# Optimization experiments

Measured on AMD Instinct MI355X. Metric: run time of the kernel, lower is better.

Reference implementation:

```python
import jax, jax.numpy as jnp
import numpy as np

PAD = 4
MAX_DISP = 4


def setup_inputs() -> dict:
    key = jax.random.key(0)
    k1, k2 = jax.random.split(key)
    in1 = jax.random.normal(k1, (8, 256, 128, 128), dtype=jnp.float32)
    in2 = jax.random.normal(k2, (8, 256, 128, 128), dtype=jnp.float32)
    return {"in1": in1, "in2": in2}


def reference(in1, in2):
    # in1, in2: [B, C, H, W]
    H, W = in1.shape[2], in1.shape[3]
    in2_pad = jnp.pad(in2, ((0, 0), (0, 0), (PAD, PAD), (PAD, PAD)))
    D = 2 * MAX_DISP + 1  # 9 displacements per axis -> 81 output channels
    outs = []
    # torch.meshgrid('ij') + zip(offsetx, offsety): dy is the outer (slow) index,
    # dx the inner (fast) index.
    for dy in range(D):
        for dx in range(D):
            # mean over channel dim of elementwise product with shifted window
            corr = jnp.mean(in1 * in2_pad[:, :, dy:dy + H, dx:dx + W],
                            axis=1, keepdims=True)  # [B,1,H,W]
            outs.append(corr)
    return jnp.concatenate(outs, axis=1)  # [B, D*D, H, W]
```

## Files before the change

kernel.cpp:

```cpp
#include <hip/hip_runtime.h>


#define B_   8
#define C_   256
#define H_   128
#define W_   128
#define ND   9
#define TY   16
#define TW   16
#define CS   (H_ * W_)
#define NST  32
#define S2SLOT 18432
#define S1SLOT 8192
#define S1OFF  55296
#define FOFF   79872
#define FAOFF  116736
#define LDS_TOTAL 133120

typedef short v8s __attribute__((ext_vector_type(8)));
typedef float v4f __attribute__((ext_vector_type(4)));

__device__ __forceinline__ unsigned short f2bf(float f) {
    union { float f; unsigned u; } v; v.f = f;
    return (unsigned short)((v.u + 0x7FFFu + ((v.u >> 16) & 1u)) >> 16);
}

__device__ __forceinline__ void dma16(const float* g, void* lds) {
    __builtin_amdgcn_global_load_lds(
        (const __attribute__((address_space(1))) void*)g,
        (__attribute__((address_space(3))) void*)lds, 16, 0, 0);
}

#define FENCE()     asm volatile("" ::: "memory")
#define WAITK2_BAR() do {                                                         \
        if (w >= 2 && w < 8) asm volatile("s_waitcnt vmcnt(2)\n\ts_barrier" ::: "memory"); \
        else                 asm volatile("s_waitcnt vmcnt(4)\n\ts_barrier" ::: "memory"); \
    } while (0)
#define WAITK1_BAR() do {                                                         \
        if (w >= 2 && w < 8) asm volatile("s_waitcnt vmcnt(1)\n\ts_barrier" ::: "memory"); \
        else                 asm volatile("s_waitcnt vmcnt(2)\n\ts_barrier" ::: "memory"); \
    } while (0)
#define WAITV0_BAR() asm volatile("s_waitcnt vmcnt(0)\n\ts_barrier" ::: "memory")
#define LGKM0_BAR()  asm volatile("s_waitcnt lgkmcnt(0)\n\ts_barrier" ::: "memory")
#define LGKM0()      asm volatile("s_waitcnt lgkmcnt(0)" ::: "memory")

__global__ __launch_bounds__(1024, 4)
void corr_mfma_kernel(const float* __restrict__ in1,
                      const float* __restrict__ in2,
                      float* __restrict__ out) {
    extern __shared__ __align__(16) char ldsbase[];
    float* S2 = (float*)ldsbase;
    float* S1 = (float*)(ldsbase + S1OFF);
    short* F  = (short*)(ldsbase + FOFF);
    short* FA = (short*)(ldsbase + FAOFF);
    float* EP = (float*)ldsbase;

    const int tid  = threadIdx.x;
    const int lane = tid & 63;
    const int w    = tid >> 6;

    const int lin = blockIdx.x;
    const int b   = lin & 7;
    const int idx = lin >> 3;
    const int x0  = (idx & 7) * TW;
    const int y0  = (idx >> 3) * TY;

    const int i_px = lane & 15;
    const int kb   = lane >> 4;

    const float* dsrc[2];
    int ddst[2];
    #pragma unroll
    for (int t = 0; t < 2; ++t) {
        if (t == 1 && w >= 2) { dsrc[t] = in2; ddst[t] = 0; continue; }
        const int q   = (w < 2) ? (w * 2 + t) : (4 + (w - 2));
        const int g   = q * 64 + lane;
        const int ch  = g / 144;
        const int rem = g % 144;
        const int r   = rem / 6;
        const int jg  = rem % 6;
        int gy = y0 - 4 + r;
        int gx = x0 - 4 + jg * 4;
        gy = gy < 0 ? 0 : (gy > H_ - 1 ? H_ - 1 : gy);
        gx = gx < 0 ? 0 : (gx > W_ - 4 ? W_ - 4 : gx);
        dsrc[t] = in2 + ((long)(b * C_) + ch) * CS + gy * W_ + gx;
        ddst[t] = q * 1024;
    }
    const float* d1src = in2;
    int d1dst = 0;
    if (w >= 8) {
        const int q   = w - 8;
        const int g   = q * 64 + lane;
        const int ch  = g >> 6;
        const int rem = g & 63;
        const int r   = rem >> 2;
        const int xg  = rem & 3;
        d1src = in1 + ((long)(b * C_) + ch) * CS + (y0 + r) * W_ + x0 + xg * 4;
        d1dst = q * 1024;
    }

    const bool c2act = (tid < 576);
    const int  crr   = tid / 24, cjj = tid % 24;
    const bool c2val = c2act && ((unsigned)(y0 - 4 + crr) < (unsigned)H_) &&
                                ((unsigned)(x0 - 4 + cjj) < (unsigned)W_);
    const bool c1act = (tid < 256);

    v4f acc0[ND];
    v4f acc1[5];
    #pragma unroll
    for (int d = 0; d < ND; ++d) acc0[d] = (v4f)0.0f;
    #pragma unroll
    for (int p = 0; p < 5; ++p)  acc1[p] = (v4f)0.0f;

#define ISSUE_G(s_) do {                                                      \
        const long so = (long)(s_) * 8 * CS;                                  \
        char* sb2 = (char*)S2 + ((s_) % 3) * S2SLOT;                          \
        dma16(dsrc[0] + so, sb2 + ddst[0]);                                   \
        if (w < 2) dma16(dsrc[1] + so, sb2 + ddst[1]);                        \
        if (w >= 8)                                                           \
            dma16(d1src + so, (char*)ldsbase + S1OFF + ((s_) % 3) * S1SLOT + d1dst); \
        FENCE();                                                              \
    } while (0)

#define CONVERT(s_) do {                                                      \
        if (c2act) {                                                          \
            const float* sh = S2 + ((s_) % 3) * 4608;                         \
            v8s pk;                                                           \
            _Pragma("unroll")                                                 \
            for (int e = 0; e < 8; ++e)                                       \
                pk[e] = (short)f2bf(sh[e * 576 + tid]);                       \
            if (!c2val) pk = (v8s)0;                                          \
            *(v8s*)&F[(((s_) & 3) * 576 + tid) * 8] = pk;                     \
        }                                                                     \
        if (c1act) {                                                          \
            const float* sa = S1 + ((s_) % 3) * 2048;                         \
            v8s pa;                                                           \
            _Pragma("unroll")                                                 \
            for (int e = 0; e < 8; ++e)                                       \
                pa[e] = (short)f2bf(sa[e * 256 + tid]);                       \
            *(v8s*)&FA[tid * 32 + ((s_) & 3) * 8] = pa;                       \
        }                                                                     \
    } while (0)

    ISSUE_G(0);
    ISSUE_G(1);
    ISSUE_G(2);
    WAITK2_BAR();
    CONVERT(0);
    LGKM0_BAR();

    #pragma unroll
    for (int s = 0; s < NST; ++s) {
        if (s + 3 < NST) ISSUE_G(s + 3);

        if ((s & 3) == 3) {
            const v8s af = *(const v8s*)&FA[w * 512 + i_px * 32 + kb * 8];
            #pragma unroll
            for (int dy = 0; dy < ND; ++dy) {
                const int rj = (w + dy) * 24 + i_px;
                const v8s f = *(const v8s*)&F[kb * 4608 + (rj << 3)];
                acc0[dy] = __builtin_amdgcn_mfma_f32_16x16x32_bf16(
                    af, f, acc0[dy], 0, 0, 0);
            }
            const int hi = i_px >> 3, j1 = 16 + (i_px & 7);
            #pragma unroll
            for (int P = 0; P < 5; ++P) {
                int r = w + 2 * P + hi;
                if (r > 23) r = 23;
                const int rj = r * 24 + j1;
                const v8s f = *(const v8s*)&F[kb * 4608 + (rj << 3)];
                acc1[P] = __builtin_amdgcn_mfma_f32_16x16x32_bf16(
                    af, f, acc1[P], 0, 0, 0);
            }
        }

        if (s + 3 < NST)       { WAITK2_BAR(); }
        else if (s == NST - 3) { WAITK1_BAR(); }
        else if (s == NST - 2) { WAITV0_BAR(); }

        if (s < NST - 1) {
            CONVERT(s + 1);
            LGKM0_BAR();
        }
    }

    float* epw = EP + w * 384;
    const int g4 = lane >> 4;
    #pragma unroll
    for (int dy = 0; dy < ND; ++dy) {
        #pragma unroll
        for (int q = 0; q < 4; ++q)
            epw[(g4 * 4 + q) * 24 + i_px] = acc0[dy][q];
        if ((i_px >> 3) == (dy & 1)) {
            #pragma unroll
            for (int q = 0; q < 4; ++q)
                epw[(g4 * 4 + q) * 24 + 16 + (i_px & 7)] = acc1[dy >> 1][q];
        }
        LGKM0();
        #pragma unroll
        for (int rep = 0; rep < 3; ++rep) {
            const int dx = g4 + rep * 4;
            if (dx < 9) {
                const float v = epw[i_px * 24 + i_px + dx] * (1.0f / 256.0f);
                out[((long)b * 81 + dy * 9 + dx) * CS + (y0 + w) * W_ + x0 + i_px] = v;
            }
        }
        LGKM0();
    }
#undef ISSUE_G
#undef CONVERT
}

extern "C" void kernel_launch(void* const* d_in, const int* in_sizes, int n_in,
                              void* d_out, int out_size, void* d_ws, size_t ws_size,
                              hipStream_t stream) {
    const float* in1 = (const float*)d_in[0];
    const float* in2 = (const float*)d_in[1];
    float* outp      = (float*)d_out;
    (void)hipFuncSetAttribute((const void*)corr_mfma_kernel,
                              hipFuncAttributeMaxDynamicSharedMemorySize,
                              LDS_TOTAL);
    corr_mfma_kernel<<<512, 1024, LDS_TOTAL, stream>>>(in1, in2, outp);
}
```

Before: 84.79 us.

## Deepen global-to-LDS prefetch to four stages and merge per-stage barriers

Moves the staging ring for in1/in2 from three to four slots, so DMA is issued four stages ahead, and grows the LDS allocation to fit. Each stage's convert step is now fenced by one combined vmcnt/lgkmcnt barrier instead of two separate barriers. An extra barrier is added only after the MFMA step that runs every fourth stage, to protect the bf16 buffers. The aim is to hide more global-load latency and cut barrier count, at the cost of nearly all the available LDS per workgroup.

```diff
diff --git a/kernel.cpp b/kernel.cpp
--- a/kernel.cpp
+++ b/kernel.cpp
@@ -12,10 +12,10 @@
 #define NST  32
 #define S2SLOT 18432
 #define S1SLOT 8192
-#define S1OFF  55296
-#define FOFF   79872
-#define FAOFF  116736
-#define LDS_TOTAL 133120
+#define S1OFF  73728
+#define FOFF   106496
+#define FAOFF  143360
+#define LDS_TOTAL 159744
 
 typedef short v8s __attribute__((ext_vector_type(8)));
 typedef float v4f __attribute__((ext_vector_type(4)));
@@ -32,16 +32,16 @@
 }
 
 #define FENCE()     asm volatile("" ::: "memory")
-#define WAITK2_BAR() do {                                                         \
-        if (w >= 2 && w < 8) asm volatile("s_waitcnt vmcnt(2)\n\ts_barrier" ::: "memory"); \
-        else                 asm volatile("s_waitcnt vmcnt(4)\n\ts_barrier" ::: "memory"); \
-    } while (0)
-#define WAITK1_BAR() do {                                                         \
-        if (w >= 2 && w < 8) asm volatile("s_waitcnt vmcnt(1)\n\ts_barrier" ::: "memory"); \
-        else                 asm volatile("s_waitcnt vmcnt(2)\n\ts_barrier" ::: "memory"); \
-    } while (0)
-#define WAITV0_BAR() asm volatile("s_waitcnt vmcnt(0)\n\ts_barrier" ::: "memory")
-#define LGKM0_BAR()  asm volatile("s_waitcnt lgkmcnt(0)\n\ts_barrier" ::: "memory")
+#define ENDK2_BAR() do {                                                          \
+        if (w >= 2 && w < 8) asm volatile("s_waitcnt vmcnt(2) lgkmcnt(0)\n\ts_barrier" ::: "memory"); \
+        else                 asm volatile("s_waitcnt vmcnt(4) lgkmcnt(0)\n\ts_barrier" ::: "memory"); \
+    } while (0)
+#define ENDK1_BAR() do {                                                          \
+        if (w >= 2 && w < 8) asm volatile("s_waitcnt vmcnt(1) lgkmcnt(0)\n\ts_barrier" ::: "memory"); \
+        else                 asm volatile("s_waitcnt vmcnt(2) lgkmcnt(0)\n\ts_barrier" ::: "memory"); \
+    } while (0)
+#define ENDK0_BAR()  asm volatile("s_waitcnt vmcnt(0) lgkmcnt(0)\n\ts_barrier" ::: "memory")
+#define LG_BAR()     asm volatile("s_waitcnt lgkmcnt(0)\n\ts_barrier" ::: "memory")
 #define LGKM0()      asm volatile("s_waitcnt lgkmcnt(0)" ::: "memory")
 
 __global__ __launch_bounds__(1024, 4)
@@ -114,17 +114,17 @@
 
 #define ISSUE_G(s_) do {                                                      \
         const long so = (long)(s_) * 8 * CS;                                  \
-        char* sb2 = (char*)S2 + ((s_) % 3) * S2SLOT;                          \
+        char* sb2 = (char*)S2 + ((s_) & 3) * S2SLOT;                          \
         dma16(dsrc[0] + so, sb2 + ddst[0]);                                   \
         if (w < 2) dma16(dsrc[1] + so, sb2 + ddst[1]);                        \
         if (w >= 8)                                                           \
-            dma16(d1src + so, (char*)ldsbase + S1OFF + ((s_) % 3) * S1SLOT + d1dst); \
+            dma16(d1src + so, (char*)ldsbase + S1OFF + ((s_) & 3) * S1SLOT + d1dst); \
         FENCE();                                                              \
     } while (0)
 
 #define CONVERT(s_) do {                                                      \
         if (c2act) {                                                          \
-            const float* sh = S2 + ((s_) % 3) * 4608;                         \
+            const float* sh = S2 + ((s_) & 3) * 4608;                         \
             v8s pk;                                                           \
             _Pragma("unroll")                                                 \
             for (int e = 0; e < 8; ++e)                                       \
@@ -133,7 +133,7 @@
             *(v8s*)&F[(((s_) & 3) * 576 + tid) * 8] = pk;                     \
         }                                                                     \
         if (c1act) {                                                          \
-            const float* sa = S1 + ((s_) % 3) * 2048;                         \
+            const float* sa = S1 + ((s_) & 3) * 2048;                         \
             v8s pa;                                                           \
             _Pragma("unroll")                                                 \
             for (int e = 0; e < 8; ++e)                                       \
@@ -145,13 +145,14 @@
     ISSUE_G(0);
     ISSUE_G(1);
     ISSUE_G(2);
-    WAITK2_BAR();
+    ISSUE_G(3);
+    ENDK2_BAR();
     CONVERT(0);
-    LGKM0_BAR();
+    LG_BAR();
 
     #pragma unroll
     for (int s = 0; s < NST; ++s) {
-        if (s + 3 < NST) ISSUE_G(s + 3);
+        if (s + 4 < NST) ISSUE_G(s + 4);
 
         if ((s & 3) == 3) {
             const v8s af = *(const v8s*)&FA[w * 512 + i_px * 32 + kb * 8];
@@ -172,16 +173,15 @@
                 acc1[P] = __builtin_amdgcn_mfma_f32_16x16x32_bf16(
                     af, f, acc1[P], 0, 0, 0);
             }
+            if (s < NST - 1) LG_BAR();
         }
 
-        if (s + 3 < NST)       { WAITK2_BAR(); }
-        else if (s == NST - 3) { WAITK1_BAR(); }
-        else if (s == NST - 2) { WAITV0_BAR(); }
-
-        if (s < NST - 1) {
-            CONVERT(s + 1);
-            LGKM0_BAR();
-        }
+        if (s < NST - 1) CONVERT(s + 1);
+
+        if (s + 4 < NST)       { ENDK2_BAR(); }
+        else if (s == NST - 4) { ENDK1_BAR(); }
+        else if (s == NST - 3) { ENDK0_BAR(); }
+        else if (s == NST - 2) { LG_BAR(); }
     }
 
     float* epw = EP + w * 384;
```

Result: no change. 83.23 us (-1.8%).
